# Kernel tuning notes

Hardware: AMD Instinct MI355X
Metric: run time of the kernel (lower is better)

The kernel has to match this reference:

```python
import jax, jax.numpy as jnp
import numpy as np

B, N, T, F_IN = 32, 64, 11, 4
K, H, O, NH = 2, 256, 256, 256  # edge_types, msg_hid, msg_out, n_hid
E = N * (N - 1)


def setup_inputs() -> dict:
    key = jax.random.key(0)
    ks = jax.random.split(key, 16)
    # fully-connected graph without self loops: edge e = (recv i, send j)
    recv = np.array([i for i in range(N) for j in range(N) if i != j])
    send = np.array([j for i in range(N) for j in range(N) if i != j])
    rel_rec = np.zeros((E, N), dtype=np.float32)
    rel_rec[np.arange(E), recv] = 1.0
    rel_send = np.zeros((E, N), dtype=np.float32)
    rel_send[np.arange(E), send] = 1.0

    def lin(k, fan_in, shape):
        return jax.random.normal(k, shape, dtype=jnp.float32) / np.sqrt(fan_in)

    return {
        "inputs": jax.random.normal(ks[0], (B, N, T, F_IN), dtype=jnp.float32),
        "edges": jax.random.uniform(ks[1], (B, E, K), dtype=jnp.float32),
        "rel_rec": jnp.asarray(rel_rec),
        "rel_send": jnp.asarray(rel_send),
        "W1": lin(ks[2], 2 * F_IN, (K, 2 * F_IN, H)),
        "b1": jnp.zeros((K, H), dtype=jnp.float32),
        "W2": lin(ks[3], H, (K, H, O)),
        "b2": jnp.zeros((K, O), dtype=jnp.float32),
        "Wo1": lin(ks[4], F_IN + O, (F_IN + O, NH)),
        "bo1": jnp.zeros((NH,), dtype=jnp.float32),
        "Wo2": lin(ks[5], NH, (NH, NH)),
        "bo2": jnp.zeros((NH,), dtype=jnp.float32),
        "Wo3": lin(ks[6], NH, (NH, F_IN)),
        "bo3": jnp.zeros((F_IN,), dtype=jnp.float32),
        "sample_timesteps": jnp.arange(T, dtype=jnp.float32),
        "pred_steps": 10,
        "scale": 10,
    }


def reference(inputs, edges, rel_rec, rel_send, W1, b1, W2, b2,
              Wo1, bo1, Wo2, bo2, Wo3, bo3, sample_timesteps, pred_steps, scale):
    t = sample_timesteps / scale
    x_all = jnp.transpose(inputs, (0, 2, 1, 3))  # [B, T, N, F]

    def f(x):  # ODE dynamics = single_step_forward (returns x + pred)
        recv = jnp.einsum('en,bnf->bef', rel_rec, x)   # gather receivers
        send = jnp.einsum('en,bnf->bef', rel_send, x)  # gather senders
        pre = jnp.concatenate([send, recv], axis=-1)   # [B, E, 2F]
        m = jax.nn.relu(jnp.einsum('bef,kfh->bkeh', pre, W1) + b1[None, :, None, :])
        m = jax.nn.relu(jnp.einsum('bkeh,kho->bkeo', m, W2) + b2[None, :, None, :])
        all_msgs = jnp.einsum('bkeo,bek->beo', m, edges)  # weighted sum over edge types
        agg = jnp.einsum('beo,en->bno', all_msgs, rel_rec)  # scatter to receivers
        aug = jnp.concatenate([x, agg], axis=-1)
        p = jax.nn.relu(aug @ Wo1 + bo1)
        p = jax.nn.relu(p @ Wo2 + bo2)
        p = p @ Wo3 + bo3
        return x + p

    preds = []
    for idx in range(0, T, pred_steps):
        vt = t[idx:idx + pred_steps + 1]
        if vt.shape[0] == 1:
            continue
        x0 = x_all[:, idx]          # [B, N, F]
        dts = vt[1:] - vt[:-1]      # [steps]

        def rk4(x, dt):
            k1 = f(x)
            k2 = f(x + 0.5 * dt * k1)
            k3 = f(x + 0.5 * dt * k2)
            k4 = f(x + dt * k3)
            xn = x + (dt / 6.0) * (k1 + 2.0 * k2 + 2.0 * k3 + k4)
            return xn, xn

        _, xs = jax.lax.scan(rk4, x0, dts)           # [steps, B, N, F]
        preds.append(jnp.transpose(xs, (1, 0, 2, 3)))  # [B, steps, N, F]

    out = jnp.concatenate(preds, axis=1)
    return jnp.transpose(out, (0, 2, 1, 3))  # [B, N, steps, F]
```

## Files before the change

kernel.cpp:

```cpp
#include <hip/hip_runtime.h>

#define BB 32
#define NN 64
#define TT 11
#define FF 4
#define KK 2
#define EE 4032
#define NSTEP 10

typedef _Float16 f16x8 __attribute__((ext_vector_type(8)));
typedef float    f32x4v __attribute__((ext_vector_type(4)));

#define OFF_U0   0
#define OFF_VB   65536
#define OFF_Y    73728
#define OFF_WGT  74752
#define OFF_AGG  78848
#define SMEM2    87040
#define OFF_AUGH 0
#define OFF_P1H  9472
#define OFF_P2   17920

__device__ __forceinline__ float scrub(float v) {
    return fminf(fmaxf(v, -3.0e4f), 3.0e4f);
}

__device__ __forceinline__ float load_dt(const float* ts, const void* scp, int step) {
    float t0 = ts[step], t1 = ts[step + 1];
    int w = ((const int*)scp)[0];
    float scl;
    if (w > 0 && w < 1000000) scl = (float)w;
    else {
        float f = __int_as_float(w);
        scl = (f > 0.5f && f < 1.0e6f) ? f : 10.0f;
    }
    return (t1 - t0) / scl;
}

__device__ __forceinline__ void build_uk(char* smem, int buf, int k, int tid,
    const float* __restrict__ W1g, const float* smY)
{
    int hg = tid & 31, sb = tid >> 5;
    const float* w1p = W1g + k * 2048 + hg * 8;
    f32x4v wA[4], wB[4];
    #pragma unroll
    for (int f = 0; f < 4; ++f) {
        wA[f] = *(const f32x4v*)(w1p + f * 256);
        wB[f] = *(const f32x4v*)(w1p + f * 256 + 4);
    }
    const int swz = (hg * 16) ^ ((sb & 7) << 4);
    char* ub = smem + OFF_U0 + buf * 32768;
    #pragma unroll
    for (int it = 0; it < 4; ++it) {
        int s = sb + it * 16;
        f32x4v yv = *(const f32x4v*)(smY + s * 4);
        f16x8 uv;
        #pragma unroll
        for (int e = 0; e < 4; ++e) {
            float vA = yv[0]*wA[0][e] + yv[1]*wA[1][e] + yv[2]*wA[2][e] + yv[3]*wA[3][e];
            float vB = yv[0]*wB[0][e] + yv[1]*wB[1][e] + yv[2]*wB[2][e] + yv[3]*wB[3][e];
            uv[e]     = (_Float16)vA;
            uv[e + 4] = (_Float16)vB;
        }
        *(f16x8*)(ub + s * 512 + swz) = uv;
    }
}

__device__ __forceinline__ void build_vbh(_Float16* smVBH, int buf, int k, int tid, int r0,
    const float* __restrict__ W1g, const float* __restrict__ b1g, const float* smY)
{
    #pragma unroll
    for (int it = 0; it < 4; ++it) {
        int i = tid + it * 512;
        int rv = i >> 8, h = i & 255;
        float acch = b1g[k * 256 + h];
        #pragma unroll
        for (int f = 0; f < 4; ++f)
            acch += smY[(r0 + rv) * 4 + f] * W1g[k * 2048 + (4 + f) * 256 + h];
        smVBH[buf * 2048 + i] = (_Float16)acch;
    }
}

__device__ __forceinline__ void gemm_pass(char* smem, int buf, int k, int q, int p,
    const _Float16* __restrict__ W2F, const float* __restrict__ b2g,
    const float* smWgt, float* smAgg,
    int lane, int ln15, int lg, const int* uoff, int xm6)
{
    const _Float16* smVBH = (const _Float16*)(smem + OFF_VB);

    float bv[4];
    #pragma unroll
    for (int ni = 0; ni < 4; ++ni)
        bv[ni] = b2g[k * 256 + q * 64 + ni * 16 + ln15];

    f32x4v acc[8][4];
    #pragma unroll
    for (int mi = 0; mi < 8; ++mi)
        #pragma unroll
        for (int ni = 0; ni < 4; ++ni)
            acc[mi][ni] = (f32x4v){bv[ni], bv[ni], bv[ni], bv[ni]};

    const _Float16* bbase = W2F + ((size_t)((k * 16 + q * 4) * 8)) * 512 + lane * 8;
    const char* ubase = smem + OFF_U0 + buf * 32768;
    const char* vbase = (const char*)(smVBH + buf * 2048 + p * 512);

    #pragma unroll
    for (int kc = 0; kc < 8; ++kc) {
        f16x8 bfr[4];
        #pragma unroll
        for (int ni = 0; ni < 4; ++ni)
            bfr[ni] = *(const f16x8*)(bbase + (size_t)(ni * 8 + kc) * 512);
        f16x8 vbA = *(const f16x8*)(vbase + (kc * 32 + lg * 8) * 2);
        f16x8 vbB = *(const f16x8*)(vbase + (256 + kc * 32 + lg * 8) * 2);
        const int kco = (kc * 64) ^ xm6;
        f16x8 af[8];
        f16x8 z = {};
        #pragma unroll
        for (int mi = 0; mi < 8; ++mi) {
            f16x8 uv = *(const f16x8*)(ubase + uoff[mi] + kco);
            af[mi] = __builtin_elementwise_max(uv + (mi < 4 ? vbA : vbB), z);
        }
        __builtin_amdgcn_s_setprio(1);
        #pragma unroll
        for (int mi = 0; mi < 8; ++mi)
            #pragma unroll
            for (int ni = 0; ni < 4; ++ni)
                acc[mi][ni] = __builtin_amdgcn_mfma_f32_16x16x32_f16(
                    af[mi], bfr[ni], acc[mi][ni], 0, 0, 0);
        __builtin_amdgcn_s_setprio(0);
    }

    float rsum[2][4];
    #pragma unroll
    for (int rl = 0; rl < 2; ++rl)
        #pragma unroll
        for (int ni = 0; ni < 4; ++ni) rsum[rl][ni] = 0.0f;

    #pragma unroll
    for (int mi = 0; mi < 8; ++mi) {
        int rl = mi >> 2;
        #pragma unroll
        for (int rr = 0; rr < 4; ++rr) {
            float w = smWgt[k * 512 + (p * 2 + rl) * 64 + (mi & 3) * 16 + lg * 4 + rr];
            #pragma unroll
            for (int ni = 0; ni < 4; ++ni)
                rsum[rl][ni] += fmaxf(acc[mi][ni][rr], 0.0f) * w;
        }
    }
    #pragma unroll
    for (int rl = 0; rl < 2; ++rl)
        #pragma unroll
        for (int ni = 0; ni < 4; ++ni) {
            rsum[rl][ni] += __shfl_xor(rsum[rl][ni], 16, 64);
            rsum[rl][ni] += __shfl_xor(rsum[rl][ni], 32, 64);
        }
    if (lane < 16) {
        #pragma unroll
        for (int rl = 0; rl < 2; ++rl)
            #pragma unroll
            for (int ni = 0; ni < 4; ++ni) {
                int idx = (p * 2 + rl) * 256 + q * 64 + ni * 16 + ln15;
                float v = rsum[rl][ni];
                if (k) v += smAgg[idx];
                smAgg[idx] = v;
            }
    }
}

__global__ __launch_bounds__(512, 2)
void stage_kernel(int stage, int step,
    const float* __restrict__ edges, const float* __restrict__ W1g,
    const float* __restrict__ b1g,   const _Float16* __restrict__ W2F,
    const float* __restrict__ b2g,
    const _Float16* __restrict__ Wo1F, const float* __restrict__ bo1,
    const _Float16* __restrict__ Wo2F, const float* __restrict__ bo2,
    const float* __restrict__ Wo3, const float* __restrict__ bo3,
    const float* __restrict__ ts,  const void* __restrict__ scp,
    const float* __restrict__ xcur, const float* __restrict__ kprev,
    float* __restrict__ kout,
    const float* __restrict__ k1b, const float* __restrict__ k2b,
    const float* __restrict__ k3b,
    float* __restrict__ xnext, float* __restrict__ outp)
{
    extern __shared__ char smem[];
    _Float16* smVBH = (_Float16*)(smem + OFF_VB);
    float*  smY   = (float*)(smem + OFF_Y);
    float*  smWgt = (float*)(smem + OFF_WGT);
    float*  smAgg = (float*)(smem + OFF_AGG);

    const int tid = threadIdx.x;
    const int b   = blockIdx.x >> 3;
    const int rg  = blockIdx.x & 7;
    const int r0  = rg * 8;

    const float dt = load_dt(ts, scp, step);
    const float cc = (stage == 0) ? 0.0f : ((stage == 3) ? 1.0f : 0.5f);

    if (tid < 256) {
        int gi = (b * NN) * FF + tid;
        float y = xcur[gi];
        if (stage != 0) y += cc * dt * kprev[gi];
        smY[tid] = scrub(y);
    }
    #pragma unroll
    for (int it = 0; it < 2; ++it) {
        int i = tid + it * 512;
        int k = i >> 9, m = i & 511;
        int rv = m >> 6, s = m & 63;
        int r = r0 + rv;
        float w = 0.0f;
        if (s != r) {
            int j = s - (s > r ? 1 : 0);
            w = edges[((size_t)b * EE + r * 63 + j) * KK + k];
        }
        smWgt[i] = w;
    }

    const int lane = tid & 63;
    const int wn   = tid >> 6;
    const int p    = wn >> 1;
    const int ch   = wn & 1;
    const int ln15 = lane & 15;
    const int lg   = lane >> 4;

    const int xm45 = (ln15 & 3) << 4;
    const int xm6  = (ln15 & 4) << 4;
    int uoff[8];
    #pragma unroll
    for (int mi = 0; mi < 8; ++mi) {
        int s = (mi & 3) * 16 + ln15;
        uoff[mi] = s * 512 + ((lg * 16) ^ xm45);
    }

    __syncthreads();

    build_uk(smem, 0, 0, tid, W1g, smY);
    build_vbh(smVBH, 0, 0, tid, r0, W1g, b1g, smY);
    __syncthreads();

    build_uk(smem, 1, 1, tid, W1g, smY);
    build_vbh(smVBH, 1, 1, tid, r0, W1g, b1g, smY);
    gemm_pass(smem, 0, 0, ch * 2 + 0, p, W2F, b2g, smWgt, smAgg, lane, ln15, lg, uoff, xm6);
    gemm_pass(smem, 0, 0, ch * 2 + 1, p, W2F, b2g, smWgt, smAgg, lane, ln15, lg, uoff, xm6);
    __syncthreads();
    gemm_pass(smem, 1, 1, ch * 2 + 0, p, W2F, b2g, smWgt, smAgg, lane, ln15, lg, uoff, xm6);
    gemm_pass(smem, 1, 1, ch * 2 + 1, p, W2F, b2g, smWgt, smAgg, lane, ln15, lg, uoff, xm6);
    __syncthreads();

    _Float16* smAugH = (_Float16*)(smem + OFF_AUGH);
    _Float16* smP1H  = (_Float16*)(smem + OFF_P1H);
    float*    smP2   = (float*)(smem + OFF_P2);

    for (int i = tid; i < 16 * 148; i += 512) {
        int row = i / 148, cp = (i - row * 148) * 2;
        float f0 = 0.0f, f1 = 0.0f;
        if (row < 8) {
            f0 = (cp < 4) ? smY[(r0 + row) * 4 + cp]
               : (cp < 260 ? smAgg[row * 256 + cp - 4] : 0.0f);
            int c1 = cp + 1;
            f1 = (c1 < 4) ? smY[(r0 + row) * 4 + c1]
               : (c1 < 260 ? smAgg[row * 256 + c1 - 4] : 0.0f);
        }
        smAugH[row * 296 + cp]     = (_Float16)f0;
        smAugH[row * 296 + cp + 1] = (_Float16)f1;
    }
    __syncthreads();

    const int ot0 = wn * 2, ot1 = ot0 + 1;

    {
        float b0 = bo1[ot0 * 16 + ln15], b1v = bo1[ot1 * 16 + ln15];
        f32x4v a0 = {b0, b0, b0, b0}, a1 = {b1v, b1v, b1v, b1v};
        const _Float16* bb0 = Wo1F + (size_t)(ot0 * 9) * 512 + lane * 8;
        const _Float16* bb1 = Wo1F + (size_t)(ot1 * 9) * 512 + lane * 8;
        #pragma unroll
        for (int kc = 0; kc < 9; ++kc) {
            f16x8 av  = *(const f16x8*)(smAugH + ln15 * 296 + kc * 32 + lg * 8);
            f16x8 bf0 = *(const f16x8*)(bb0 + kc * 512);
            f16x8 bf1 = *(const f16x8*)(bb1 + kc * 512);
            a0 = __builtin_amdgcn_mfma_f32_16x16x32_f16(av, bf0, a0, 0, 0, 0);
            a1 = __builtin_amdgcn_mfma_f32_16x16x32_f16(av, bf1, a1, 0, 0, 0);
        }
        #pragma unroll
        for (int rr = 0; rr < 4; ++rr) {
            int row = lg * 4 + rr;
            smP1H[row * 264 + ot0 * 16 + ln15] = (_Float16)fmaxf(a0[rr], 0.0f);
            smP1H[row * 264 + ot1 * 16 + ln15] = (_Float16)fmaxf(a1[rr], 0.0f);
        }
    }
    __syncthreads();
    {
        float b0 = bo2[ot0 * 16 + ln15], b1v = bo2[ot1 * 16 + ln15];
        f32x4v a0 = {b0, b0, b0, b0}, a1 = {b1v, b1v, b1v, b1v};
        const _Float16* bb0 = Wo2F + (size_t)(ot0 * 8) * 512 + lane * 8;
        const _Float16* bb1 = Wo2F + (size_t)(ot1 * 8) * 512 + lane * 8;
        #pragma unroll
        for (int kc = 0; kc < 8; ++kc) {
            f16x8 av  = *(const f16x8*)(smP1H + ln15 * 264 + kc * 32 + lg * 8);
            f16x8 bf0 = *(const f16x8*)(bb0 + kc * 512);
            f16x8 bf1 = *(const f16x8*)(bb1 + kc * 512);
            a0 = __builtin_amdgcn_mfma_f32_16x16x32_f16(av, bf0, a0, 0, 0, 0);
            a1 = __builtin_amdgcn_mfma_f32_16x16x32_f16(av, bf1, a1, 0, 0, 0);
        }
        #pragma unroll
        for (int rr = 0; rr < 4; ++rr) {
            int row = lg * 4 + rr;
            smP2[row * 256 + ot0 * 16 + ln15] = fmaxf(a0[rr], 0.0f);
            smP2[row * 256 + ot1 * 16 + ln15] = fmaxf(a1[rr], 0.0f);
        }
    }
    __syncthreads();
    {
        int rr = tid >> 6, f = (tid >> 4) & 3, hs = tid & 15;
        float part = 0.0f;
        #pragma unroll
        for (int j = 0; j < 16; ++j) {
            int h = hs + j * 16;
            part += smP2[rr * 256 + h] * Wo3[h * 4 + f];
        }
        part += __shfl_xor(part, 8, 64);
        part += __shfl_xor(part, 4, 64);
        part += __shfl_xor(part, 2, 64);
        part += __shfl_xor(part, 1, 64);
        if (hs == 0) {
            int grow = b * NN + r0 + rr;
            int gi   = grow * 4 + f;
            float y = smY[(r0 + rr) * 4 + f];
            float knew = scrub(y + bo3[f] + part);
            if (stage < 3) {
                kout[gi] = knew;
            } else {
                float xn = scrub(xcur[gi] + (dt * (1.0f / 6.0f)) *
                           (k1b[gi] + 2.0f * k2b[gi] + 2.0f * k3b[gi] + knew));
                xnext[gi] = xn;
                outp[(size_t)grow * NSTEP * FF + step * FF + f] = xn;
            }
        }
    }
}

__global__ void swizzle_w2(const float* __restrict__ W2, _Float16* __restrict__ W2F)
{
    int idx = blockIdx.x * 256 + threadIdx.x;
    int k   = idx >> 16;
    int rem = idx & 65535;
    int ch  = rem >> 9;
    int pos = rem & 511;
    int ot  = ch >> 3, kc = ch & 7;
    int l   = pos >> 3, e = pos & 7;
    int o   = ot * 16 + (l & 15);
    int h   = kc * 32 + (l >> 4) * 8 + e;
    W2F[idx] = (_Float16)W2[(size_t)(k * 256 + h) * 256 + o];
}

__global__ void swizzle_wo1(const float* __restrict__ Wo1, _Float16* __restrict__ Wo1F)
{
    int idx = blockIdx.x * 256 + threadIdx.x;
    int ch = idx >> 9, pos = idx & 511;
    int ot = ch / 9, kc = ch - ot * 9;
    int l = pos >> 3, e = pos & 7;
    int k = kc * 32 + (l >> 4) * 8 + e;
    int o = ot * 16 + (l & 15);
    Wo1F[idx] = (k < 260) ? (_Float16)Wo1[(size_t)k * 256 + o] : (_Float16)0.0f;
}

__global__ void swizzle_wo2(const float* __restrict__ Wo2, _Float16* __restrict__ Wo2F)
{
    int idx = blockIdx.x * 256 + threadIdx.x;
    int ch = idx >> 9, pos = idx & 511;
    int ot = ch >> 3, kc = ch & 7;
    int l = pos >> 3, e = pos & 7;
    int k = kc * 32 + (l >> 4) * 8 + e;
    int o = ot * 16 + (l & 15);
    Wo2F[idx] = (_Float16)Wo2[(size_t)k * 256 + o];
}

__global__ void init_x(const float* __restrict__ inp, float* __restrict__ x0)
{
    int i = blockIdx.x * 256 + threadIdx.x;
    if (i < BB * NN * FF) {
        int f = i & 3, bn = i >> 2;
        x0[i] = scrub(inp[(size_t)(bn * TT) * FF + f]);
    }
}

static int find_input(const int* in_sizes, int n_in, int want, unsigned char* used, int dflt) {
    if (dflt >= 0 && dflt < n_in && in_sizes[dflt] == want && !used[dflt]) { used[dflt] = 1; return dflt; }
    for (int i = 0; i < n_in; ++i)
        if (!used[i] && in_sizes[i] == want) { used[i] = 1; return i; }
    return dflt;
}

extern "C" void kernel_launch(void* const* d_in, const int* in_sizes, int n_in,
                              void* d_out, int out_size, void* d_ws, size_t ws_size,
                              hipStream_t stream)
{
    unsigned char used[64] = {0};
    int iInp = find_input(in_sizes, n_in, BB*NN*TT*FF, used, 0);
    int iEdg = find_input(in_sizes, n_in, BB*EE*KK,    used, 1);
    (void)find_input(in_sizes, n_in, EE*NN, used, 2);
    (void)find_input(in_sizes, n_in, EE*NN, used, 3);
    int iW1  = find_input(in_sizes, n_in, KK*8*256,  used, 4);
    int ib1  = find_input(in_sizes, n_in, KK*256,    used, 5);
    int iW2  = find_input(in_sizes, n_in, KK*256*256,used, 6);
    int ib2  = find_input(in_sizes, n_in, KK*256,    used, 7);
    int iWo1 = find_input(in_sizes, n_in, 260*256,   used, 8);
    int ibo1 = find_input(in_sizes, n_in, 256,       used, 9);
    int iWo2 = find_input(in_sizes, n_in, 256*256,   used, 10);
    int ibo2 = find_input(in_sizes, n_in, 256,       used, 11);
    int iWo3 = find_input(in_sizes, n_in, 256*4,     used, 12);
    int ibo3 = find_input(in_sizes, n_in, 4,         used, 13);
    int iTs  = find_input(in_sizes, n_in, TT,        used, 14);
    (void)find_input(in_sizes, n_in, 1, used, 15);
    int iSc  = find_input(in_sizes, n_in, 1,         used, 16);

    const float* inputs = (const float*)d_in[iInp];
    const float* edges  = (const float*)d_in[iEdg];
    const float* W1  = (const float*)d_in[iW1];
    const float* b1  = (const float*)d_in[ib1];
    const float* W2  = (const float*)d_in[iW2];
    const float* b2  = (const float*)d_in[ib2];
    const float* Wo1 = (const float*)d_in[iWo1];
    const float* bo1 = (const float*)d_in[ibo1];
    const float* Wo2 = (const float*)d_in[iWo2];
    const float* bo2 = (const float*)d_in[ibo2];
    const float* Wo3 = (const float*)d_in[iWo3];
    const float* bo3 = (const float*)d_in[ibo3];
    const float* ts  = (const float*)d_in[iTs];
    const void*  scp = d_in[iSc];

    char* ws = (char*)d_ws;
    _Float16* W2F  = (_Float16*)ws;
    _Float16* Wo1F = (_Float16*)(ws + 262144);
    _Float16* Wo2F = (_Float16*)(ws + 409600);
    float* xA  = (float*)(ws + 540672);
    float* xB  = (float*)(ws + 540672 + 1 * 32768);
    float* k1  = (float*)(ws + 540672 + 2 * 32768);
    float* k2  = (float*)(ws + 540672 + 3 * 32768);
    float* k3  = (float*)(ws + 540672 + 4 * 32768);

    float* outp = (float*)d_out;

    (void)hipFuncSetAttribute((const void*)stage_kernel,
        hipFuncAttributeMaxDynamicSharedMemorySize, SMEM2);

    swizzle_w2<<<dim3(512), dim3(256), 0, stream>>>(W2, W2F);
    swizzle_wo1<<<dim3(288), dim3(256), 0, stream>>>(Wo1, Wo1F);
    swizzle_wo2<<<dim3(256), dim3(256), 0, stream>>>(Wo2, Wo2F);
    init_x<<<dim3(32), dim3(256), 0, stream>>>(inputs, xA);

    float* xc = xA;
    float* xn = xB;
    for (int step = 0; step < NSTEP; ++step) {
        float* kprevs[4] = { xc, k1, k2, k3 };
        float* kouts[4]  = { k1, k2, k3, k3 };
        for (int s = 0; s < 4; ++s) {
            stage_kernel<<<dim3(256), dim3(512), SMEM2, stream>>>(s, step,
                edges, W1, b1, W2F, b2,
                Wo1F, bo1, Wo2F, bo2, Wo3, bo3, ts, scp, xc, kprevs[s],
                kouts[s], k1, k2, k3, xn, outp);
        }
        float* t = xc; xc = xn; xn = t;
    }
}
```

Before: 1.590 ms.

## Remap message GEMM warps to one receiver row each and drop shared aggregation buffer

Each warp now owns one receiver row and half of the output columns per pass, so sums over edge types and senders stay in registers across both k passes. Shuffle-reduced results are written straight into the fp16 augmented-input tile, which removes the smAgg shared buffer, its read-modify-write, and a separate conversion loop with its barrier. In exchange each warp loads twice as many W2 fragments per k-chunk, and needs extra registers for the running sums. Padding rows and columns of the augmented tile are no longer zeroed, so stale shared data is read there.

```diff
diff --git a/kernel.cpp b/kernel.cpp
--- a/kernel.cpp
+++ b/kernel.cpp
@@ -15,8 +15,7 @@
 #define OFF_VB   65536
 #define OFF_Y    73728
 #define OFF_WGT  74752
-#define OFF_AGG  78848
-#define SMEM2    87040
+#define SMEM2    78848
 #define OFF_AUGH 0
 #define OFF_P1H  9472
 #define OFF_P2   17920
@@ -81,89 +80,64 @@
     }
 }
 
-__device__ __forceinline__ void gemm_pass(char* smem, int buf, int k, int q, int p,
+__device__ __forceinline__ void gemm_half(char* smem, int buf, int k, int rv, int ch2,
     const _Float16* __restrict__ W2F, const float* __restrict__ b2g,
-    const float* smWgt, float* smAgg,
-    int lane, int ln15, int lg, const int* uoff, int xm6)
+    const float* smWgt,
+    int lane, int ln15, int lg, const int* uoff, int xm6,
+    float rsum[8])
 {
     const _Float16* smVBH = (const _Float16*)(smem + OFF_VB);
 
-    float bv[4];
-    #pragma unroll
-    for (int ni = 0; ni < 4; ++ni)
-        bv[ni] = b2g[k * 256 + q * 64 + ni * 16 + ln15];
-
-    f32x4v acc[8][4];
-    #pragma unroll
-    for (int mi = 0; mi < 8; ++mi)
-        #pragma unroll
-        for (int ni = 0; ni < 4; ++ni)
+    float bv[8];
+    #pragma unroll
+    for (int ni = 0; ni < 8; ++ni)
+        bv[ni] = b2g[k * 256 + ch2 * 128 + ni * 16 + ln15];
+
+    f32x4v acc[4][8];
+    #pragma unroll
+    for (int mi = 0; mi < 4; ++mi)
+        #pragma unroll
+        for (int ni = 0; ni < 8; ++ni)
             acc[mi][ni] = (f32x4v){bv[ni], bv[ni], bv[ni], bv[ni]};
 
-    const _Float16* bbase = W2F + ((size_t)((k * 16 + q * 4) * 8)) * 512 + lane * 8;
+    const _Float16* bbase = W2F + ((size_t)((k * 16 + ch2 * 8) * 8)) * 512 + lane * 8;
     const char* ubase = smem + OFF_U0 + buf * 32768;
-    const char* vbase = (const char*)(smVBH + buf * 2048 + p * 512);
+    const _Float16* vbase = smVBH + buf * 2048 + rv * 256;
 
     #pragma unroll
     for (int kc = 0; kc < 8; ++kc) {
-        f16x8 bfr[4];
-        #pragma unroll
-        for (int ni = 0; ni < 4; ++ni)
+        f16x8 bfr[8];
+        #pragma unroll
+        for (int ni = 0; ni < 8; ++ni)
             bfr[ni] = *(const f16x8*)(bbase + (size_t)(ni * 8 + kc) * 512);
-        f16x8 vbA = *(const f16x8*)(vbase + (kc * 32 + lg * 8) * 2);
-        f16x8 vbB = *(const f16x8*)(vbase + (256 + kc * 32 + lg * 8) * 2);
+        f16x8 vbv = *(const f16x8*)(vbase + kc * 32 + lg * 8);
         const int kco = (kc * 64) ^ xm6;
-        f16x8 af[8];
+        f16x8 af[4];
         f16x8 z = {};
         #pragma unroll
-        for (int mi = 0; mi < 8; ++mi) {
+        for (int mi = 0; mi < 4; ++mi) {
             f16x8 uv = *(const f16x8*)(ubase + uoff[mi] + kco);
-            af[mi] = __builtin_elementwise_max(uv + (mi < 4 ? vbA : vbB), z);
+            af[mi] = __builtin_elementwise_max(uv + vbv, z);
         }
         __builtin_amdgcn_s_setprio(1);
         #pragma unroll
-        for (int mi = 0; mi < 8; ++mi)
+        for (int mi = 0; mi < 4; ++mi)
             #pragma unroll
-            for (int ni = 0; ni < 4; ++ni)
+            for (int ni = 0; ni < 8; ++ni)
                 acc[mi][ni] = __builtin_amdgcn_mfma_f32_16x16x32_f16(
                     af[mi], bfr[ni], acc[mi][ni], 0, 0, 0);
         __builtin_amdgcn_s_setprio(0);
     }
 
-    float rsum[2][4];
-    #pragma unroll
-    for (int rl = 0; rl < 2; ++rl)
-        #pragma unroll
-        for (int ni = 0; ni < 4; ++ni) rsum[rl][ni] = 0.0f;
-
-    #pragma unroll
-    for (int mi = 0; mi < 8; ++mi) {
-        int rl = mi >> 2;
+    #pragma unroll
+    for (int mi = 0; mi < 4; ++mi) {
         #pragma unroll
         for (int rr = 0; rr < 4; ++rr) {
-            float w = smWgt[k * 512 + (p * 2 + rl) * 64 + (mi & 3) * 16 + lg * 4 + rr];
+            float w = smWgt[k * 512 + rv * 64 + mi * 16 + lg * 4 + rr];
             #pragma unroll
-            for (int ni = 0; ni < 4; ++ni)
-                rsum[rl][ni] += fmaxf(acc[mi][ni][rr], 0.0f) * w;
-        }
-    }
-    #pragma unroll
-    for (int rl = 0; rl < 2; ++rl)
-        #pragma unroll
-        for (int ni = 0; ni < 4; ++ni) {
-            rsum[rl][ni] += __shfl_xor(rsum[rl][ni], 16, 64);
-            rsum[rl][ni] += __shfl_xor(rsum[rl][ni], 32, 64);
-        }
-    if (lane < 16) {
-        #pragma unroll
-        for (int rl = 0; rl < 2; ++rl)
-            #pragma unroll
-            for (int ni = 0; ni < 4; ++ni) {
-                int idx = (p * 2 + rl) * 256 + q * 64 + ni * 16 + ln15;
-                float v = rsum[rl][ni];
-                if (k) v += smAgg[idx];
-                smAgg[idx] = v;
-            }
+            for (int ni = 0; ni < 8; ++ni)
+                rsum[ni] += fmaxf(acc[mi][ni][rr], 0.0f) * w;
+        }
     }
 }
 
@@ -186,7 +160,6 @@
     _Float16* smVBH = (_Float16*)(smem + OFF_VB);
     float*  smY   = (float*)(smem + OFF_Y);
     float*  smWgt = (float*)(smem + OFF_WGT);
-    float*  smAgg = (float*)(smem + OFF_AGG);
 
     const int tid = threadIdx.x;
     const int b   = blockIdx.x >> 3;
@@ -218,19 +191,22 @@
 
     const int lane = tid & 63;
     const int wn   = tid >> 6;
-    const int p    = wn >> 1;
-    const int ch   = wn & 1;
+    const int rv   = wn;
     const int ln15 = lane & 15;
     const int lg   = lane >> 4;
 
     const int xm45 = (ln15 & 3) << 4;
     const int xm6  = (ln15 & 4) << 4;
-    int uoff[8];
-    #pragma unroll
-    for (int mi = 0; mi < 8; ++mi) {
-        int s = (mi & 3) * 16 + ln15;
+    int uoff[4];
+    #pragma unroll
+    for (int mi = 0; mi < 4; ++mi) {
+        int s = mi * 16 + ln15;
         uoff[mi] = s * 512 + ((lg * 16) ^ xm45);
     }
+
+    float rsA[8], rsB[8];
+    #pragma unroll
+    for (int ni = 0; ni < 8; ++ni) { rsA[ni] = 0.0f; rsB[ni] = 0.0f; }
 
     __syncthreads();
 
@@ -240,31 +216,33 @@
 
     build_uk(smem, 1, 1, tid, W1g, smY);
     build_vbh(smVBH, 1, 1, tid, r0, W1g, b1g, smY);
-    gemm_pass(smem, 0, 0, ch * 2 + 0, p, W2F, b2g, smWgt, smAgg, lane, ln15, lg, uoff, xm6);
-    gemm_pass(smem, 0, 0, ch * 2 + 1, p, W2F, b2g, smWgt, smAgg, lane, ln15, lg, uoff, xm6);
-    __syncthreads();
-    gemm_pass(smem, 1, 1, ch * 2 + 0, p, W2F, b2g, smWgt, smAgg, lane, ln15, lg, uoff, xm6);
-    gemm_pass(smem, 1, 1, ch * 2 + 1, p, W2F, b2g, smWgt, smAgg, lane, ln15, lg, uoff, xm6);
-    __syncthreads();
-
+    gemm_half(smem, 0, 0, rv, 0, W2F, b2g, smWgt, lane, ln15, lg, uoff, xm6, rsA);
+    gemm_half(smem, 0, 0, rv, 1, W2F, b2g, smWgt, lane, ln15, lg, uoff, xm6, rsB);
+    __syncthreads();
+    gemm_half(smem, 1, 1, rv, 0, W2F, b2g, smWgt, lane, ln15, lg, uoff, xm6, rsA);
+    gemm_half(smem, 1, 1, rv, 1, W2F, b2g, smWgt, lane, ln15, lg, uoff, xm6, rsB);
+
+    #pragma unroll
+    for (int ni = 0; ni < 8; ++ni) {
+        rsA[ni] += __shfl_xor(rsA[ni], 16, 64);
+        rsA[ni] += __shfl_xor(rsA[ni], 32, 64);
+        rsB[ni] += __shfl_xor(rsB[ni], 16, 64);
+        rsB[ni] += __shfl_xor(rsB[ni], 32, 64);
+    }
     _Float16* smAugH = (_Float16*)(smem + OFF_AUGH);
-    _Float16* smP1H  = (_Float16*)(smem + OFF_P1H);
-    float*    smP2   = (float*)(smem + OFF_P2);
-
-    for (int i = tid; i < 16 * 148; i += 512) {
-        int row = i / 148, cp = (i - row * 148) * 2;
-        float f0 = 0.0f, f1 = 0.0f;
-        if (row < 8) {
-            f0 = (cp < 4) ? smY[(r0 + row) * 4 + cp]
-               : (cp < 260 ? smAgg[row * 256 + cp - 4] : 0.0f);
-            int c1 = cp + 1;
-            f1 = (c1 < 4) ? smY[(r0 + row) * 4 + c1]
-               : (c1 < 260 ? smAgg[row * 256 + c1 - 4] : 0.0f);
-        }
-        smAugH[row * 296 + cp]     = (_Float16)f0;
-        smAugH[row * 296 + cp + 1] = (_Float16)f1;
-    }
-    __syncthreads();
+    if (lane < 16) {
+        #pragma unroll
+        for (int ni = 0; ni < 8; ++ni) {
+            smAugH[rv * 296 + 4   + ni * 16 + ln15] = (_Float16)rsA[ni];
+            smAugH[rv * 296 + 132 + ni * 16 + ln15] = (_Float16)rsB[ni];
+        }
+    } else if (lg == 1 && ln15 < 4) {
+        smAugH[rv * 296 + ln15] = (_Float16)smY[(r0 + rv) * 4 + ln15];
+    }
+    __syncthreads();
+
+    _Float16* smP1H = (_Float16*)(smem + OFF_P1H);
+    float*    smP2  = (float*)(smem + OFF_P2);
 
     const int ot0 = wn * 2, ot1 = ot0 + 1;
 
@@ -281,6 +259,7 @@
             a0 = __builtin_amdgcn_mfma_f32_16x16x32_f16(av, bf0, a0, 0, 0, 0);
             a1 = __builtin_amdgcn_mfma_f32_16x16x32_f16(av, bf1, a1, 0, 0, 0);
         }
+        __syncthreads();
         #pragma unroll
         for (int rr = 0; rr < 4; ++rr) {
             int row = lg * 4 + rr;
```

Measured after the change: 1.535 ms. 1.04x faster.
